# Optimization experiments

Hardware: AMD Instinct MI355X
Metric: run time of the kernel (lower is better)

## Reference

```python
import jax, jax.numpy as jnp
import numpy as np

NOVELTY_THRESHOLD = 0.5  # cfg.novelty_threshold
NUM_ENVS, MEM_SIZE, FEAT = 1024, 200, 512


def setup_inputs() -> dict:
    key = jax.random.key(0)
    k1, k2, k3, k4, k5 = jax.random.split(key, 5)
    memory = jax.random.normal(k1, (NUM_ENVS, MEM_SIZE, FEAT), dtype=jnp.float32)
    obs_features = jax.random.normal(k2, (NUM_ENVS, FEAT), dtype=jnp.float32)
    similarities = jax.random.uniform(k3, (NUM_ENVS,), dtype=jnp.float32)
    mem_mask = jax.random.randint(k4, (NUM_ENVS,), 0, MEM_SIZE + 1, dtype=jnp.int64 if jax.config.jax_enable_x64 else jnp.int32)
    rand_idx = jax.random.randint(k5, (NUM_ENVS,), 0, MEM_SIZE, dtype=mem_mask.dtype)
    return {
        "memory": memory,
        "obs_features": obs_features,
        "similarities": similarities,
        "mem_mask": mem_mask,
        "rand_idx": rand_idx,
    }


def reference(memory, obs_features, similarities, mem_mask, rand_idx):
    """Vectorized equivalent of ReachabilityPolicy.add_to_memory.

    memory:       [E, M, D] per-env episodic memory bank
    obs_features: [E, D]    new feature per env
    similarities: [E]       similarity score per env
    mem_mask:     [E]       number of valid slots per env (0..M)
    rand_idx:     [E]       random replacement slot when memory is full
    Returns (updated_memory, updated_mem_mask).
    """
    E, M, D = memory.shape
    add_mask = similarities > NOVELTY_THRESHOLD          # [E] bool: write this env?
    full_mem = mem_mask == M                              # [E] bool: bank full?
    # counter only grows for non-full envs that accept the new feature
    mem_mask_new = mem_mask + ((~full_mem) & add_mask).astype(mem_mask.dtype)
    # full envs replace a random slot; non-full envs append at (new_count - 1).
    # (clamp to 0 for the no-write case where mem_mask_new - 1 == -1; the
    #  jnp.where below restores the original row there so it is a no-op.)
    add_idx = jnp.where(full_mem, rand_idx, jnp.maximum(mem_mask_new - 1, 0))  # [E]
    env_ids = jnp.arange(E)
    old_rows = memory[env_ids, add_idx]                   # [E, D]
    new_rows = jnp.where(add_mask[:, None], obs_features, old_rows)
    memory_new = memory.at[env_ids, add_idx].set(new_rows)
    return memory_new, mem_mask_new
```

## Files before the change

### kernel.cpp

```cpp
#include <hip/hip_runtime.h>
#include <hip/hip_bf16.h>

constexpr int E = 1024;
constexpr int M = 200;
constexpr int D = 512;
constexpr long long TOT = (long long)E * M * D;
constexpr int N4 = (int)(TOT / 4);
constexpr int PER_ENV4 = M * D / 4;
constexpr int PER_ROW4 = D / 4;
constexpr float NOVELTY_THRESHOLD = 0.5f;

__global__ __launch_bounds__(256) void reach_update(
    const float4* __restrict__ mem,
    const float4* __restrict__ obs,
    const float*  __restrict__ sim,
    const int*    __restrict__ mask,
    const int*    __restrict__ ridx,
    float4*       __restrict__ out_mem,
    float*        __restrict__ out_mask
) {
    int i4 = blockIdx.x * blockDim.x + threadIdx.x;
    if (i4 >= N4) return;

    int e    = i4 / PER_ENV4;
    int rem  = i4 - e * PER_ENV4;
    int row  = rem >> 7;
    int col4 = rem & (PER_ROW4 - 1);

    float s   = sim[e];
    int   mk  = mask[e];
    bool  add  = s > NOVELTY_THRESHOLD;
    bool  full = (mk == M);
    int   nm   = mk + ((!full) && add ? 1 : 0);
    int   am1  = nm - 1; if (am1 < 0) am1 = 0;
    int   idx  = full ? ridx[e] : am1;

    float4 v = mem[i4];
    if (add && row == idx) {
        v = obs[e * PER_ROW4 + col4];
    }
    out_mem[i4] = v;

    if (i4 < E) {
        int   mk2   = mask[i4];
        bool  add2  = sim[i4] > NOVELTY_THRESHOLD;
        bool  full2 = (mk2 == M);
        int   nm2   = mk2 + ((!full2) && add2 ? 1 : 0);
        out_mask[i4] = (float)nm2;
    }
}

extern "C" void kernel_launch(void* const* d_in, const int* in_sizes, int n_in,
                              void* d_out, int out_size, void* d_ws, size_t ws_size,
                              hipStream_t stream) {
    const float4* mem  = (const float4*)d_in[0];
    const float4* obs  = (const float4*)d_in[1];
    const float*  sim  = (const float*)d_in[2];
    const int*    mask = (const int*)d_in[3];
    const int*    ridx = (const int*)d_in[4];

    float* out      = (float*)d_out;
    float* out_mask = out + TOT;

    constexpr int BLOCK = 256;
    int grid = (N4 + BLOCK - 1) / BLOCK;
    reach_update<<<grid, BLOCK, 0, stream>>>(mem, obs, sim, mask, ridx,
                                             (float4*)out, out_mask);
}
```

Measured before the change: 646.2 us.

## Replace fused copy kernel with device memcpy plus per-env row fixup kernel

The full memory bank is now copied with hipMemcpyAsync, and a small kernel with one block per env writes only the replaced row and the new mask. Before, a single elementwise kernel did the copy and computed the select condition for every element. The aim is to use the runtime's tuned device-to-device copy path in place of a custom copy loop. It adds a second launch and an ordering dependency on the stream, and it depends on how fast the memcpy engine or blit kernel is compared with the custom kernel.

```diff
diff --git a/kernel.cpp b/kernel.cpp
--- a/kernel.cpp
+++ b/kernel.cpp
@@ -5,13 +5,11 @@
 constexpr int M = 200;
 constexpr int D = 512;
 constexpr long long TOT = (long long)E * M * D;
-constexpr int N4 = (int)(TOT / 4);
 constexpr int PER_ENV4 = M * D / 4;
 constexpr int PER_ROW4 = D / 4;
 constexpr float NOVELTY_THRESHOLD = 0.5f;
 
-__global__ __launch_bounds__(256) void reach_update(
-    const float4* __restrict__ mem,
+__global__ __launch_bounds__(128) void reach_fixup(
     const float4* __restrict__ obs,
     const float*  __restrict__ sim,
     const int*    __restrict__ mask,
@@ -19,41 +17,27 @@
     float4*       __restrict__ out_mem,
     float*        __restrict__ out_mask
 ) {
-    int i4 = blockIdx.x * blockDim.x + threadIdx.x;
-    if (i4 >= N4) return;
+    int e = blockIdx.x;
+    int t = threadIdx.x;
 
-    int e    = i4 / PER_ENV4;
-    int rem  = i4 - e * PER_ENV4;
-    int row  = rem >> 7;
-    int col4 = rem & (PER_ROW4 - 1);
+    int  mk   = mask[e];
+    bool add  = sim[e] > NOVELTY_THRESHOLD;
+    bool full = (mk == M);
+    int  nm   = mk + (int)((!full) && add);
 
-    float s   = sim[e];
-    int   mk  = mask[e];
-    bool  add  = s > NOVELTY_THRESHOLD;
-    bool  full = (mk == M);
-    int   nm   = mk + ((!full) && add ? 1 : 0);
-    int   am1  = nm - 1; if (am1 < 0) am1 = 0;
-    int   idx  = full ? ridx[e] : am1;
+    if (t == 0) out_mask[e] = (float)nm;
 
-    float4 v = mem[i4];
-    if (add && row == idx) {
-        v = obs[e * PER_ROW4 + col4];
-    }
-    out_mem[i4] = v;
-
-    if (i4 < E) {
-        int   mk2   = mask[i4];
-        bool  add2  = sim[i4] > NOVELTY_THRESHOLD;
-        bool  full2 = (mk2 == M);
-        int   nm2   = mk2 + ((!full2) && add2 ? 1 : 0);
-        out_mask[i4] = (float)nm2;
+    if (add) {
+        int idx = full ? ridx[e] : (nm - 1);
+        out_mem[(long long)e * PER_ENV4 + (long long)idx * PER_ROW4 + t] =
+            obs[e * PER_ROW4 + t];
     }
 }
 
 extern "C" void kernel_launch(void* const* d_in, const int* in_sizes, int n_in,
                               void* d_out, int out_size, void* d_ws, size_t ws_size,
                               hipStream_t stream) {
-    const float4* mem  = (const float4*)d_in[0];
+    const void*   mem  = d_in[0];
     const float4* obs  = (const float4*)d_in[1];
     const float*  sim  = (const float*)d_in[2];
     const int*    mask = (const int*)d_in[3];
@@ -62,8 +46,9 @@
     float* out      = (float*)d_out;
     float* out_mask = out + TOT;
 
-    constexpr int BLOCK = 256;
-    int grid = (N4 + BLOCK - 1) / BLOCK;
-    reach_update<<<grid, BLOCK, 0, stream>>>(mem, obs, sim, mask, ridx,
-                                             (float4*)out, out_mask);
+    hipMemcpyAsync(out, mem, (size_t)TOT * sizeof(float),
+                   hipMemcpyDeviceToDevice, stream);
+
+    reach_fixup<<<E, 128, 0, stream>>>(obs, sim, mask, ridx,
+                                       (float4*)out, out_mask);
 }
```

After: 669.1 us. 3.5% more time.
